# Kernel optimization log

Hardware: AMD Instinct MI355X
Metric: run time of the kernel (lower is better)

The kernel has to match this reference:

```python
import jax, jax.numpy as jnp
import numpy as np

B, H, L, D = 8, 16, 1024, 64


def setup_inputs() -> dict:
    key = jax.random.key(0)
    kq, kk, kv, kb, km = jax.random.split(key, 5)
    q = jax.random.normal(kq, (B, H, L, D), dtype=jnp.float32)
    k = jax.random.normal(kk, (B, H, L, D), dtype=jnp.float32)
    v = jax.random.normal(kv, (B, H, L, D), dtype=jnp.float32)
    # relative-position bias, broadcast over batch
    bias = jax.random.normal(kb, (1, H, L, L), dtype=jnp.float32)
    # variable-length padding mask: each sequence has length in [L//2, L]
    lengths = jax.random.randint(km, (B,), L // 2, L + 1)
    mask = jnp.arange(L)[None, :] < lengths[:, None]  # [B, L] bool
    return {"q": q, "k": k, "v": v, "mask": mask, "bias": bias}


def reference(q, k, v, mask, bias):
    # dots: [b h m n]; NOTE: source computes self.scale but never applies it
    dots = jnp.einsum('bhmd,bhnd->bhmn', q, k) + bias
    # mask[:, None, None, :] & mask[:, None, :, None]
    m2 = mask[:, None, None, :] & mask[:, None, :, None]  # [b 1 m n]
    neg = jnp.finfo(dots.dtype).min
    probs = jax.nn.softmax(jnp.where(m2, dots, neg), axis=-1)
    probs = jnp.where(m2, probs, jnp.zeros((), dtype=probs.dtype))  # XSoftmax zeroing
    # dropout is identity in eval mode
    context = jnp.einsum('bhmn,bhnd->bhmd', probs, v)
    b, h, m, d = context.shape
    return context.transpose(0, 2, 1, 3).reshape(b, m, h * d)  # [b m (h d)]
```

## Files before the change

### kernel.cpp

```cpp
#include <hip/hip_runtime.h>
#include <hip/hip_bf16.h>

#define B_ 8
#define H_ 16
#define L_ 1024
#define D_ 64

typedef __attribute__((ext_vector_type(8))) short short8;
typedef __attribute__((ext_vector_type(4))) short short4v;
typedef __attribute__((ext_vector_type(4))) float floatx4;

__device__ inline short bf16s(float f) {
    union { float f; unsigned u; } un; un.f = f;
    unsigned u = un.u;
    u += 0x7FFFu + ((u >> 16) & 1u);
    return (short)(u >> 16);
}
__device__ inline float bf16f(unsigned short u) {
    union { unsigned u; float f; } un; un.u = ((unsigned)u) << 16;
    return un.f;
}

__device__ inline floatx4 mfma16(short8 a, short8 b, floatx4 c) {
    return __builtin_amdgcn_mfma_f32_16x16x32_bf16(a, b, c, 0, 0, 0);
}

#define KSTR 72
#define VSTR 40
#define PSTR 40
#define KPL (32 * KSTR)
#define VPL (64 * VSTR)
#define PPL (16 * PSTR)

__launch_bounds__(256, 4)
__global__ void prep_kernel(const float* __restrict__ k,
                            const float* __restrict__ v,
                            unsigned short* __restrict__ khi,
                            unsigned short* __restrict__ klo,
                            unsigned short* __restrict__ vth) {
    __shared__ alignas(16) short vt[64 * 72];
    const int bid = blockIdx.x;
    const int kt  = bid & 15;
    const int h   = (bid >> 4) & 15;
    const int b   = bid >> 8;
    const int tid = threadIdx.x;
    const size_t base = ((size_t)(b * H_ + h) * L_ + kt * 64) * D_;

    #pragma unroll
    for (int i = 0; i < 4; i++) {
        const int idx = (i * 256 + tid) * 4;
        const float4 f = *(const float4*)(k + base + idx);
        short4v hi, lo;
        hi[0] = bf16s(f.x); lo[0] = bf16s(f.x - bf16f((unsigned short)hi[0]));
        hi[1] = bf16s(f.y); lo[1] = bf16s(f.y - bf16f((unsigned short)hi[1]));
        hi[2] = bf16s(f.z); lo[2] = bf16s(f.z - bf16f((unsigned short)hi[2]));
        hi[3] = bf16s(f.w); lo[3] = bf16s(f.w - bf16f((unsigned short)hi[3]));
        *(short4v*)(khi + base + idx) = hi;
        *(short4v*)(klo + base + idx) = lo;
    }

    #pragma unroll
    for (int i = 0; i < 4; i++) {
        const int idx = (i * 256 + tid) * 4;
        const int key = idx >> 6;
        const int d0  = idx & 63;
        const float4 f = *(const float4*)(v + base + idx);
        vt[(d0 + 0) * 72 + key] = bf16s(f.x);
        vt[(d0 + 1) * 72 + key] = bf16s(f.y);
        vt[(d0 + 2) * 72 + key] = bf16s(f.z);
        vt[(d0 + 3) * 72 + key] = bf16s(f.w);
    }
    __syncthreads();
    #pragma unroll
    for (int i = 0; i < 2; i++) {
        const int s = i * 2048 + tid * 8;
        const int d = s >> 6;
        const int kk = s & 63;
        short8 r = *(const short8*)&vt[d * 72 + kk];
        *(short8*)(vth + ((size_t)((b * H_ + h) * D_) + d) * L_ + kt * 64 + kk) = r;
    }
}

__launch_bounds__(256, 2)
__global__ void attn_fast(const float* __restrict__ q,
                          const unsigned short* __restrict__ khi,
                          const unsigned short* __restrict__ klo,
                          const unsigned short* __restrict__ vth,
                          const void* __restrict__ mask,
                          const float* __restrict__ bias,
                          float* __restrict__ out) {
    __shared__ alignas(16) short lds_k[2 * 2 * 2 * KPL];
    __shared__ alignas(16) short lds_vt[2 * 2 * VPL];
    __shared__ alignas(16) short lds_p[4 * PPL];
    __shared__ int s_len;

    const int bid  = blockIdx.x;
    const int b    = (bid >> 3) & 7;
    const int p_   = ((bid >> 6) << 3) | (bid & 7);
    const int h    = p_ >> 4;
    const int mt   = p_ & 15;
    const int tid  = threadIdx.x;
    const int wave = tid >> 6;
    const int lane = tid & 63;
    const int l16  = lane & 15;
    const int quad = lane >> 4;
    short* lds_pw = lds_p + wave * PPL;

    if (tid == 0) s_len = 0;
    __syncthreads();
    {
        const unsigned char* mb = (const unsigned char*)mask;
        int fmt;
        if (mb[0] == 1 && mb[1] != 0)      fmt = 0;
        else if (mb[0] == 1)               fmt = 1;
        else if (mb[1] != 0)               fmt = 2;
        else                               fmt = 1;
        int s = 0;
        if (fmt == 0) {
            const unsigned char* r = mb + b * L_;
            #pragma unroll
            for (int i = 0; i < 4; i++) s += (r[tid * 4 + i] != 0);
        } else if (fmt == 1) {
            const unsigned int* r = (const unsigned int*)mask + b * L_;
            #pragma unroll
            for (int i = 0; i < 4; i++) s += (r[tid * 4 + i] != 0u);
        } else {
            const unsigned short* r = (const unsigned short*)mask + b * L_;
            #pragma unroll
            for (int i = 0; i < 4; i++) s += (r[tid * 4 + i] != 0);
        }
        #pragma unroll
        for (int off = 32; off; off >>= 1) s += __shfl_down(s, off);
        if (lane == 0) atomicAdd(&s_len, s);
    }
    __syncthreads();
    const int len = s_len;

    const int m_base = mt * 64 + wave * 16;
    const float* qp = q + ((size_t)((b * H_ + h) * L_) + (m_base + l16)) * D_;
    short8 qh[2], ql[2];
    #pragma unroll
    for (int c = 0; c < 2; c++)
        #pragma unroll
        for (int j = 0; j < 8; j++) {
            float x = qp[c * 32 + quad * 8 + j];
            short hh = bf16s(x);
            qh[c][j] = hh;
            ql[c][j] = bf16s(x - bf16f((unsigned short)hh));
        }

    floatx4 acc[4];
    float l_p[4];
    #pragma unroll
    for (int c = 0; c < 4; c++) { acc[c][0] = acc[c][1] = acc[c][2] = acc[c][3] = 0.f; }
    #pragma unroll
    for (int r = 0; r < 4; r++) l_p[r] = 0.f;

    const size_t kvoff = (size_t)((b * H_ + h) * L_) * D_;
    const size_t vtoff = (size_t)((b * H_ + h) * D_) * L_;
    const float* bias_base = bias + (size_t)h * L_ * L_
                           + (size_t)(m_base + quad * 4) * L_ + l16;

    const int ntiles = (len + 31) >> 5;
    const int npairs = (ntiles + 1) >> 1;

    const int key_s = tid >> 3;
    const int d_s   = (tid & 7) * 8;
    const int dv    = tid >> 2;
    const int k8v   = (tid & 3) * 8;

    short8 khA, klA, vvA, khB, klB, vvB;
    short8 pfA, pfB;
    short8 vfA0, vfA1, vfA2, vfA3, vfB0, vfB1, vfB2, vfB3;

    {
        const size_t ksrc = kvoff + (size_t)tid * 8;
        khA = *(const short8*)(khi + ksrc);
        klA = *(const short8*)(klo + ksrc);
        khB = *(const short8*)(khi + ksrc + 32 * D_);
        klB = *(const short8*)(klo + ksrc + 32 * D_);
        vvA = *(const short8*)(vth + vtoff + (size_t)dv * L_ + k8v);
        vvB = *(const short8*)(vth + vtoff + (size_t)dv * L_ + 32 + k8v);
        short* kA = lds_k;
        short* kB = lds_k + 2 * KPL;
        *(short8*)&kA[key_s * KSTR + d_s] = khA;
        *(short8*)&kA[KPL + key_s * KSTR + d_s] = klA;
        *(short8*)&kB[key_s * KSTR + d_s] = khB;
        *(short8*)&kB[KPL + key_s * KSTR + d_s] = klB;
        *(short8*)&lds_vt[dv * VSTR + k8v] = vvA;
        *(short8*)&lds_vt[VPL + dv * VSTR + k8v] = vvB;
    }
    __syncthreads();

    for (int p = 0; p < npairs; p++) {
        const int n0  = p * 64;
        const int par = p & 1;
        short* kbA = lds_k + (par * 2 + 0) * (2 * KPL);
        short* kbB = lds_k + (par * 2 + 1) * (2 * KPL);
        short* vbA = lds_vt + (par * 2 + 0) * VPL;
        short* vbB = lds_vt + (par * 2 + 1) * VPL;
        const bool pfetch = (p + 1 < npairs);

        if (p > 0) {
            __builtin_amdgcn_s_setprio(1);
            acc[0] = mfma16(pfA, vfA0, acc[0]);
            acc[1] = mfma16(pfA, vfA1, acc[1]);
            acc[2] = mfma16(pfA, vfA2, acc[2]);
            acc[3] = mfma16(pfA, vfA3, acc[3]);
            acc[0] = mfma16(pfB, vfB0, acc[0]);
            acc[1] = mfma16(pfB, vfB1, acc[1]);
            acc[2] = mfma16(pfB, vfB2, acc[2]);
            acc[3] = mfma16(pfB, vfB3, acc[3]);
            __builtin_amdgcn_s_setprio(0);
        }

        if (pfetch) {
            const size_t ksrc = kvoff + (size_t)(n0 + 64) * D_ + (size_t)tid * 8;
            khA = *(const short8*)(khi + ksrc);
            klA = *(const short8*)(klo + ksrc);
            khB = *(const short8*)(khi + ksrc + 32 * D_);
            klB = *(const short8*)(klo + ksrc + 32 * D_);
            vvA = *(const short8*)(vth + vtoff + (size_t)dv * L_ + (n0 + 64) + k8v);
            vvB = *(const short8*)(vth + vtoff + (size_t)dv * L_ + (n0 + 96) + k8v);
        }

        float bc[16];
        #pragma unroll
        for (int r = 0; r < 4; r++) {
            bc[2 * r]         = bias_base[(size_t)r * L_ + n0];
            bc[2 * r + 1]     = bias_base[(size_t)r * L_ + n0 + 16];
            bc[8 + 2 * r]     = bias_base[(size_t)r * L_ + n0 + 32];
            bc[8 + 2 * r + 1] = bias_base[(size_t)r * L_ + n0 + 48];
        }

        vfA0 = *(const short8*)&vbA[(0 * 16 + l16) * VSTR + quad * 8];
        vfA1 = *(const short8*)&vbA[(1 * 16 + l16) * VSTR + quad * 8];
        vfA2 = *(const short8*)&vbA[(2 * 16 + l16) * VSTR + quad * 8];
        vfA3 = *(const short8*)&vbA[(3 * 16 + l16) * VSTR + quad * 8];
        vfB0 = *(const short8*)&vbB[(0 * 16 + l16) * VSTR + quad * 8];
        vfB1 = *(const short8*)&vbB[(1 * 16 + l16) * VSTR + quad * 8];
        vfB2 = *(const short8*)&vbB[(2 * 16 + l16) * VSTR + quad * 8];
        vfB3 = *(const short8*)&vbB[(3 * 16 + l16) * VSTR + quad * 8];

        floatx4 s0a, s1a, s0b, s1b;
        s0a[0]=s0a[1]=s0a[2]=s0a[3]=0.f;
        s1a[0]=s1a[1]=s1a[2]=s1a[3]=0.f;
        s0b[0]=s0b[1]=s0b[2]=s0b[3]=0.f;
        s1b[0]=s1b[1]=s1b[2]=s1b[3]=0.f;
        __builtin_amdgcn_s_setprio(1);
        #pragma unroll
        for (int c = 0; c < 2; c++) {
            const int o0 = l16 * KSTR + c * 32 + quad * 8;
            const int o1 = (16 + l16) * KSTR + c * 32 + quad * 8;
            short8 a0h = *(const short8*)&kbA[o0];
            short8 a1h = *(const short8*)&kbA[o1];
            short8 a0l = *(const short8*)&kbA[KPL + o0];
            short8 a1l = *(const short8*)&kbA[KPL + o1];
            short8 b0h = *(const short8*)&kbB[o0];
            short8 b1h = *(const short8*)&kbB[o1];
            short8 b0l = *(const short8*)&kbB[KPL + o0];
            short8 b1l = *(const short8*)&kbB[KPL + o1];
            s0a = mfma16(qh[c], a0h, s0a);
            s0b = mfma16(qh[c], b0h, s0b);
            s1a = mfma16(qh[c], a1h, s1a);
            s1b = mfma16(qh[c], b1h, s1b);
            s0a = mfma16(ql[c], a0h, s0a);
            s0b = mfma16(ql[c], b0h, s0b);
            s1a = mfma16(ql[c], a1h, s1a);
            s1b = mfma16(ql[c], b1h, s1b);
            s0a = mfma16(qh[c], a0l, s0a);
            s0b = mfma16(qh[c], b0l, s0b);
            s1a = mfma16(qh[c], a1l, s1a);
            s1b = mfma16(qh[c], b1l, s1b);
        }
        __builtin_amdgcn_s_setprio(0);

        #pragma unroll
        for (int r = 0; r < 4; r++) {
            s0a[r] += bc[2 * r];     s1a[r] += bc[2 * r + 1];
            s0b[r] += bc[8 + 2 * r]; s1b[r] += bc[8 + 2 * r + 1];
        }
        if (n0 + l16      >= len) { s0a[0]=s0a[1]=s0a[2]=s0a[3] = -1e30f; }
        if (n0 + 16 + l16 >= len) { s1a[0]=s1a[1]=s1a[2]=s1a[3] = -1e30f; }
        if (n0 + 32 + l16 >= len) { s0b[0]=s0b[1]=s0b[2]=s0b[3] = -1e30f; }
        if (n0 + 48 + l16 >= len) { s1b[0]=s1b[1]=s1b[2]=s1b[3] = -1e30f; }

        #pragma unroll
        for (int r = 0; r < 4; r++) {
            const float p0 = __expf(fminf(s0a[r], 60.f));
            const float p1 = __expf(fminf(s1a[r], 60.f));
            l_p[r] += p0 + p1;
            const int row = quad * 4 + r;
            lds_pw[row * PSTR + l16]      = bf16s(p0);
            lds_pw[row * PSTR + 16 + l16] = bf16s(p1);
        }
        pfA = *(const short8*)&lds_pw[l16 * PSTR + quad * 8];
        #pragma unroll
        for (int r = 0; r < 4; r++) {
            const float p0 = __expf(fminf(s0b[r], 60.f));
            const float p1 = __expf(fminf(s1b[r], 60.f));
            l_p[r] += p0 + p1;
            const int row = quad * 4 + r;
            lds_pw[row * PSTR + l16]      = bf16s(p0);
            lds_pw[row * PSTR + 16 + l16] = bf16s(p1);
        }
        pfB = *(const short8*)&lds_pw[l16 * PSTR + quad * 8];

        if (pfetch) {
            const int par2 = par ^ 1;
            short* kA2 = lds_k + (par2 * 2 + 0) * (2 * KPL);
            short* kB2 = lds_k + (par2 * 2 + 1) * (2 * KPL);
            short* vA2 = lds_vt + (par2 * 2 + 0) * VPL;
            short* vB2 = lds_vt + (par2 * 2 + 1) * VPL;
            *(short8*)&kA2[key_s * KSTR + d_s] = khA;
            *(short8*)&kA2[KPL + key_s * KSTR + d_s] = klA;
            *(short8*)&kB2[key_s * KSTR + d_s] = khB;
            *(short8*)&kB2[KPL + key_s * KSTR + d_s] = klB;
            *(short8*)&vA2[dv * VSTR + k8v] = vvA;
            *(short8*)&vB2[dv * VSTR + k8v] = vvB;
        }
        __syncthreads();
    }

    {
        __builtin_amdgcn_s_setprio(1);
        acc[0] = mfma16(pfA, vfA0, acc[0]);
        acc[1] = mfma16(pfA, vfA1, acc[1]);
        acc[2] = mfma16(pfA, vfA2, acc[2]);
        acc[3] = mfma16(pfA, vfA3, acc[3]);
        acc[0] = mfma16(pfB, vfB0, acc[0]);
        acc[1] = mfma16(pfB, vfB1, acc[1]);
        acc[2] = mfma16(pfB, vfB2, acc[2]);
        acc[3] = mfma16(pfB, vfB3, acc[3]);
        __builtin_amdgcn_s_setprio(0);
    }

    #pragma unroll
    for (int r = 0; r < 4; r++) {
        float ls = l_p[r];
        #pragma unroll
        for (int off = 8; off; off >>= 1) ls += __shfl_xor(ls, off);
        const int mg = m_base + quad * 4 + r;
        const bool valid = (mg < len);
        const float invl = (ls > 0.f) ? (1.0f / ls) : 0.f;
        float* op = out + (size_t)(b * L_ + mg) * (H_ * D_) + h * D_;
        #pragma unroll
        for (int c = 0; c < 4; c++)
            op[c * 16 + l16] = valid ? acc[c][r] * invl : 0.f;
    }
}

__launch_bounds__(256, 4)
__global__ void attn_fallback(const float* __restrict__ q,
                              const float* __restrict__ k,
                              const float* __restrict__ v,
                              const void* __restrict__ mask,
                              const float* __restrict__ bias,
                              float* __restrict__ out) {
    __shared__ alignas(16) short lds_k[2 * KPL];
    __shared__ alignas(16) short lds_vt[2 * VPL];
    __shared__ alignas(16) short lds_p[4 * 2 * PPL];
    __shared__ int s_len;

    const int bid  = blockIdx.x;
    const int mt   = bid & 15;
    const int h    = (bid >> 4) & 15;
    const int b    = bid >> 8;
    const int tid  = threadIdx.x;
    const int wave = tid >> 6;
    const int lane = tid & 63;
    const int l16  = lane & 15;
    const int quad = lane >> 4;
    short* lds_pw = lds_p + wave * (2 * PPL);

    if (tid == 0) s_len = 0;
    __syncthreads();
    {
        const unsigned char* mb = (const unsigned char*)mask;
        int fmt;
        if (mb[0] == 1 && mb[1] != 0)      fmt = 0;
        else if (mb[0] == 1)               fmt = 1;
        else if (mb[1] != 0)               fmt = 2;
        else                               fmt = 1;
        int s = 0;
        if (fmt == 0) {
            const unsigned char* r = mb + b * L_;
            for (int i = 0; i < 4; i++) s += (r[tid * 4 + i] != 0);
        } else if (fmt == 1) {
            const unsigned int* r = (const unsigned int*)mask + b * L_;
            for (int i = 0; i < 4; i++) s += (r[tid * 4 + i] != 0u);
        } else {
            const unsigned short* r = (const unsigned short*)mask + b * L_;
            for (int i = 0; i < 4; i++) s += (r[tid * 4 + i] != 0);
        }
        for (int off = 32; off; off >>= 1) s += __shfl_down(s, off);
        if (lane == 0) atomicAdd(&s_len, s);
    }
    __syncthreads();
    const int len = s_len;

    const int m_base = mt * 64 + wave * 16;
    const float* qp = q + ((size_t)((b * H_ + h) * L_) + (m_base + l16)) * D_;
    short8 qh[2], ql[2];
    for (int c = 0; c < 2; c++)
        for (int j = 0; j < 8; j++) {
            float x = qp[c * 32 + quad * 8 + j];
            short hh = bf16s(x);
            qh[c][j] = hh;
            ql[c][j] = bf16s(x - bf16f((unsigned short)hh));
        }

    floatx4 acc[4];
    float m_i[4], l_i[4];
    for (int c = 0; c < 4; c++) { acc[c][0]=acc[c][1]=acc[c][2]=acc[c][3]=0.f; }
    for (int r = 0; r < 4; r++) { m_i[r] = -1e30f; l_i[r] = 0.f; }

    const size_t kvoff = (size_t)((b * H_ + h) * L_) * D_;
    const size_t boff0 = (size_t)h * L_ * L_;
    const int ntiles = (len + 31) >> 5;

    for (int kt = 0; kt < ntiles; kt++) {
        const int n0 = kt * 32;
        __syncthreads();
        {
            const int e0  = tid * 8;
            const int key = e0 >> 6;
            const int d0  = e0 & 63;
            const float* ksrc = k + kvoff + (size_t)(n0 + key) * D_ + d0;
            const float* vsrc = v + kvoff + (size_t)(n0 + key) * D_ + d0;
            short* kdh = &lds_k[key * KSTR + d0];
            for (int i = 0; i < 8; i++) {
                float x = ksrc[i];
                short hh = bf16s(x);
                kdh[i]       = hh;
                kdh[KPL + i] = bf16s(x - bf16f((unsigned short)hh));
            }
            for (int i = 0; i < 8; i++) {
                float x = vsrc[i];
                short hh = bf16s(x);
                lds_vt[(d0 + i) * VSTR + key]       = hh;
                lds_vt[VPL + (d0 + i) * VSTR + key] = bf16s(x - bf16f((unsigned short)hh));
            }
        }
        __syncthreads();

        floatx4 s0, s1;
        s0[0]=s0[1]=s0[2]=s0[3]=0.f;
        s1[0]=s1[1]=s1[2]=s1[3]=0.f;
        for (int c = 0; c < 2; c++) {
            const int o0 = l16 * KSTR + c * 32 + quad * 8;
            const int o1 = (16 + l16) * KSTR + c * 32 + quad * 8;
            short8 k0h = *(const short8*)&lds_k[o0];
            short8 k1h = *(const short8*)&lds_k[o1];
            short8 k0l = *(const short8*)&lds_k[KPL + o0];
            short8 k1l = *(const short8*)&lds_k[KPL + o1];
            s0 = mfma16(qh[c], k0h, s0);
            s0 = mfma16(ql[c], k0h, s0);
            s0 = mfma16(qh[c], k0l, s0);
            s1 = mfma16(qh[c], k1h, s1);
            s1 = mfma16(ql[c], k1h, s1);
            s1 = mfma16(qh[c], k1l, s1);
        }

        for (int r = 0; r < 4; r++) {
            const float* bp = bias + boff0 + (size_t)(m_base + quad * 4 + r) * L_ + n0;
            s0[r] += bp[l16];
            s1[r] += bp[16 + l16];
        }
        if (n0 + l16      >= len) { s0[0]=s0[1]=s0[2]=s0[3] = -1e30f; }
        if (n0 + 16 + l16 >= len) { s1[0]=s1[1]=s1[2]=s1[3] = -1e30f; }

        for (int r = 0; r < 4; r++) {
            float mx = fmaxf(s0[r], s1[r]);
            for (int off = 8; off; off >>= 1) mx = fmaxf(mx, __shfl_xor(mx, off));
            const float mnew  = fmaxf(m_i[r], mx);
            const float alpha = __expf(m_i[r] - mnew);
            const float p0 = __expf(s0[r] - mnew);
            const float p1 = __expf(s1[r] - mnew);
            float ps = p0 + p1;
            for (int off = 8; off; off >>= 1) ps += __shfl_xor(ps, off);
            l_i[r] = l_i[r] * alpha + ps;
            m_i[r] = mnew;
            for (int c = 0; c < 4; c++) acc[c][r] *= alpha;
            const int row = quad * 4 + r;
            short h0 = bf16s(p0), h1 = bf16s(p1);
            lds_pw[row * PSTR + l16]      = h0;
            lds_pw[row * PSTR + 16 + l16] = h1;
            lds_pw[PPL + row * PSTR + l16]      = bf16s(p0 - bf16f((unsigned short)h0));
            lds_pw[PPL + row * PSTR + 16 + l16] = bf16s(p1 - bf16f((unsigned short)h1));
        }

        short8 pfh = *(const short8*)&lds_pw[l16 * PSTR + quad * 8];
        short8 pfl = *(const short8*)&lds_pw[PPL + l16 * PSTR + quad * 8];
        for (int c = 0; c < 4; c++) {
            const int vo = (c * 16 + l16) * VSTR + quad * 8;
            short8 vfh = *(const short8*)&lds_vt[vo];
            short8 vfl = *(const short8*)&lds_vt[VPL + vo];
            acc[c] = mfma16(pfh, vfh, acc[c]);
            acc[c] = mfma16(pfl, vfh, acc[c]);
            acc[c] = mfma16(pfh, vfl, acc[c]);
        }
    }

    for (int r = 0; r < 4; r++) {
        const int mg = m_base + quad * 4 + r;
        const bool valid = (mg < len);
        const float invl = (l_i[r] > 0.f) ? (1.0f / l_i[r]) : 0.f;
        float* op = out + (size_t)(b * L_ + mg) * (H_ * D_) + h * D_;
        for (int c = 0; c < 4; c++)
            op[c * 16 + l16] = valid ? acc[c][r] * invl : 0.f;
    }
}

extern "C" void kernel_launch(void* const* d_in, const int* in_sizes, int n_in,
                              void* d_out, int out_size, void* d_ws, size_t ws_size,
                              hipStream_t stream) {
    const float* q    = (const float*)d_in[0];
    const float* k    = (const float*)d_in[1];
    const float* v    = (const float*)d_in[2];
    const void*  mask = d_in[3];
    const float* bias = (const float*)d_in[4];
    float* out = (float*)d_out;

    const size_t PLANE = (size_t)B_ * H_ * L_ * D_;
    const size_t need  = 3 * PLANE * sizeof(unsigned short);

    dim3 grid(B_ * H_ * (L_ / 64));
    if (ws_size >= need) {
        unsigned short* khi = (unsigned short*)d_ws;
        unsigned short* klo = khi + PLANE;
        unsigned short* vth = klo + PLANE;
        prep_kernel<<<grid, 256, 0, stream>>>(k, v, khi, klo, vth);
        attn_fast<<<grid, 256, 0, stream>>>(q, khi, klo, vth, mask, bias, out);
    } else {
        attn_fallback<<<grid, 256, 0, stream>>>(q, k, v, mask, bias, out);
    }
}
```

Baseline: 290.4 us.

## Use 512-thread blocks covering 128 query rows to share K/V tiles

The attention kernel now runs 8 waves per block, so each block covers 128 query rows and the grid is halved. Each staged 64-key K (hi/lo) and V tile is loaded once per block by all 512 threads and shared by twice as many waves, which halves global-to-LDS traffic per query row. The LDS layout changes to single 64-key buffers with a new V stride. The costs are larger block-wide barriers, fewer blocks in flight, and more LDS per block. Register pressure from the new launch bounds may also become a problem.

```diff
diff --git a/kernel.cpp b/kernel.cpp
--- a/kernel.cpp
+++ b/kernel.cpp
@@ -31,6 +31,9 @@
 #define KPL (32 * KSTR)
 #define VPL (64 * VSTR)
 #define PPL (16 * PSTR)
+#define KPL64 (64 * KSTR)
+#define VSTR2 68
+#define VPL64 (64 * VSTR2)
 
 __launch_bounds__(256, 4)
 __global__ void prep_kernel(const float* __restrict__ k,
@@ -81,7 +84,7 @@
     }
 }
 
-__launch_bounds__(256, 2)
+__launch_bounds__(512, 4)
 __global__ void attn_fast(const float* __restrict__ q,
                           const unsigned short* __restrict__ khi,
                           const unsigned short* __restrict__ klo,
@@ -89,16 +92,16 @@
                           const void* __restrict__ mask,
                           const float* __restrict__ bias,
                           float* __restrict__ out) {
-    __shared__ alignas(16) short lds_k[2 * 2 * 2 * KPL];
-    __shared__ alignas(16) short lds_vt[2 * 2 * VPL];
-    __shared__ alignas(16) short lds_p[4 * PPL];
+    __shared__ alignas(16) short lds_k[2 * 2 * KPL64];
+    __shared__ alignas(16) short lds_vt[2 * VPL64];
+    __shared__ alignas(16) short lds_p[8 * PPL];
     __shared__ int s_len;
 
     const int bid  = blockIdx.x;
     const int b    = (bid >> 3) & 7;
     const int p_   = ((bid >> 6) << 3) | (bid & 7);
-    const int h    = p_ >> 4;
-    const int mt   = p_ & 15;
+    const int h    = p_ >> 3;
+    const int mt2  = p_ & 7;
     const int tid  = threadIdx.x;
     const int wave = tid >> 6;
     const int lane = tid & 63;
@@ -108,7 +111,7 @@
 
     if (tid == 0) s_len = 0;
     __syncthreads();
-    {
+    if (tid < 256) {
         const unsigned char* mb = (const unsigned char*)mask;
         int fmt;
         if (mb[0] == 1 && mb[1] != 0)      fmt = 0;
@@ -136,7 +139,7 @@
     __syncthreads();
     const int len = s_len;
 
-    const int m_base = mt * 64 + wave * 16;
+    const int m_base = mt2 * 128 + wave * 16;
     const float* qp = q + ((size_t)((b * H_ + h) * L_) + (m_base + l16)) * D_;
     short8 qh[2], ql[2];
     #pragma unroll
@@ -166,39 +169,29 @@
 
     const int key_s = tid >> 3;
     const int d_s   = (tid & 7) * 8;
-    const int dv    = tid >> 2;
-    const int k8v   = (tid & 3) * 8;
-
-    short8 khA, klA, vvA, khB, klB, vvB;
+    const int dv    = tid >> 3;
+    const int k8v   = (tid & 7) * 8;
+
+    short8 kh_r, kl_r, vv_r;
     short8 pfA, pfB;
     short8 vfA0, vfA1, vfA2, vfA3, vfB0, vfB1, vfB2, vfB3;
 
     {
         const size_t ksrc = kvoff + (size_t)tid * 8;
-        khA = *(const short8*)(khi + ksrc);
-        klA = *(const short8*)(klo + ksrc);
-        khB = *(const short8*)(khi + ksrc + 32 * D_);
-        klB = *(const short8*)(klo + ksrc + 32 * D_);
-        vvA = *(const short8*)(vth + vtoff + (size_t)dv * L_ + k8v);
-        vvB = *(const short8*)(vth + vtoff + (size_t)dv * L_ + 32 + k8v);
-        short* kA = lds_k;
-        short* kB = lds_k + 2 * KPL;
-        *(short8*)&kA[key_s * KSTR + d_s] = khA;
-        *(short8*)&kA[KPL + key_s * KSTR + d_s] = klA;
-        *(short8*)&kB[key_s * KSTR + d_s] = khB;
-        *(short8*)&kB[KPL + key_s * KSTR + d_s] = klB;
-        *(short8*)&lds_vt[dv * VSTR + k8v] = vvA;
-        *(short8*)&lds_vt[VPL + dv * VSTR + k8v] = vvB;
+        kh_r = *(const short8*)(khi + ksrc);
+        kl_r = *(const short8*)(klo + ksrc);
+        vv_r = *(const short8*)(vth + vtoff + (size_t)dv * L_ + k8v);
+        *(short8*)&lds_k[key_s * KSTR + d_s] = kh_r;
+        *(short8*)&lds_k[KPL64 + key_s * KSTR + d_s] = kl_r;
+        *(short8*)&lds_vt[dv * VSTR2 + k8v] = vv_r;
     }
     __syncthreads();
 
     for (int p = 0; p < npairs; p++) {
         const int n0  = p * 64;
         const int par = p & 1;
-        short* kbA = lds_k + (par * 2 + 0) * (2 * KPL);
-        short* kbB = lds_k + (par * 2 + 1) * (2 * KPL);
-        short* vbA = lds_vt + (par * 2 + 0) * VPL;
-        short* vbB = lds_vt + (par * 2 + 1) * VPL;
+        short* kb = lds_k + par * (2 * KPL64);
+        short* vb = lds_vt + par * VPL64;
         const bool pfetch = (p + 1 < npairs);
 
         if (p > 0) {
@@ -216,12 +209,9 @@
 
         if (pfetch) {
             const size_t ksrc = kvoff + (size_t)(n0 + 64) * D_ + (size_t)tid * 8;
-            khA = *(const short8*)(khi + ksrc);
-            klA = *(const short8*)(klo + ksrc);
-            khB = *(const short8*)(khi + ksrc + 32 * D_);
-            klB = *(const short8*)(klo + ksrc + 32 * D_);
-            vvA = *(const short8*)(vth + vtoff + (size_t)dv * L_ + (n0 + 64) + k8v);
-            vvB = *(const short8*)(vth + vtoff + (size_t)dv * L_ + (n0 + 96) + k8v);
+            kh_r = *(const short8*)(khi + ksrc);
+            kl_r = *(const short8*)(klo + ksrc);
+            vv_r = *(const short8*)(vth + vtoff + (size_t)dv * L_ + (n0 + 64) + k8v);
         }
 
         float bc[16];
@@ -233,14 +223,14 @@
             bc[8 + 2 * r + 1] = bias_base[(size_t)r * L_ + n0 + 48];
         }
 
-        vfA0 = *(const short8*)&vbA[(0 * 16 + l16) * VSTR + quad * 8];
-        vfA1 = *(const short8*)&vbA[(1 * 16 + l16) * VSTR + quad * 8];
-        vfA2 = *(const short8*)&vbA[(2 * 16 + l16) * VSTR + quad * 8];
-        vfA3 = *(const short8*)&vbA[(3 * 16 + l16) * VSTR + quad * 8];
-        vfB0 = *(const short8*)&vbB[(0 * 16 + l16) * VSTR + quad * 8];
-        vfB1 = *(const short8*)&vbB[(1 * 16 + l16) * VSTR + quad * 8];
-        vfB2 = *(const short8*)&vbB[(2 * 16 + l16) * VSTR + quad * 8];
-        vfB3 = *(const short8*)&vbB[(3 * 16 + l16) * VSTR + quad * 8];
+        vfA0 = *(const short8*)&vb[(0 * 16 + l16) * VSTR2 + quad * 8];
+        vfA1 = *(const short8*)&vb[(1 * 16 + l16) * VSTR2 + quad * 8];
+        vfA2 = *(const short8*)&vb[(2 * 16 + l16) * VSTR2 + quad * 8];
+        vfA3 = *(const short8*)&vb[(3 * 16 + l16) * VSTR2 + quad * 8];
+        vfB0 = *(const short8*)&vb[(0 * 16 + l16) * VSTR2 + 32 + quad * 8];
+        vfB1 = *(const short8*)&vb[(1 * 16 + l16) * VSTR2 + 32 + quad * 8];
+        vfB2 = *(const short8*)&vb[(2 * 16 + l16) * VSTR2 + 32 + quad * 8];
+        vfB3 = *(const short8*)&vb[(3 * 16 + l16) * VSTR2 + 32 + quad * 8];
 
         floatx4 s0a, s1a, s0b, s1b;
         s0a[0]=s0a[1]=s0a[2]=s0a[3]=0.f;
@@ -250,16 +240,18 @@
         __builtin_amdgcn_s_setprio(1);
         #pragma unroll
         for (int c = 0; c < 2; c++) {
-            const int o0 = l16 * KSTR + c * 32 + quad * 8;
-            const int o1 = (16 + l16) * KSTR + c * 32 + quad * 8;
-            short8 a0h = *(const short8*)&kbA[o0];
-            short8 a1h = *(const short8*)&kbA[o1];
-            short8 a0l = *(const short8*)&kbA[KPL + o0];
-            short8 a1l = *(const short8*)&kbA[KPL + o1];
-            short8 b0h = *(const short8*)&kbB[o0];
-            short8 b1h = *(const short8*)&kbB[o1];
-            short8 b0l = *(const short8*)&kbB[KPL + o0];
-            short8 b1l = *(const short8*)&kbB[KPL + o1];
+            const int o0  = l16 * KSTR + c * 32 + quad * 8;
+            const int o1  = (16 + l16) * KSTR + c * 32 + quad * 8;
+            const int o0b = (32 + l16) * KSTR + c * 32 + quad * 8;
+            const int o1b = (48 + l16) * KSTR + c * 32 + quad * 8;
+            short8 a0h = *(const short8*)&kb[o0];
+            short8 a1h = *(const short8*)&kb[o1];
+            short8 a0l = *(const short8*)&kb[KPL64 + o0];
+            short8 a1l = *(const short8*)&kb[KPL64 + o1];
+            short8 b0h = *(const short8*)&kb[o0b];
+            short8 b1h = *(const short8*)&kb[o1b];
+            short8 b0l = *(const short8*)&kb[KPL64 + o0b];
+            short8 b1l = *(const short8*)&kb[KPL64 + o1b];
             s0a = mfma16(qh[c], a0h, s0a);
             s0b = mfma16(qh[c], b0h, s0b);
             s1a = mfma16(qh[c], a1h, s1a);
@@ -308,16 +300,11 @@
 
         if (pfetch) {
             const int par2 = par ^ 1;
-            short* kA2 = lds_k + (par2 * 2 + 0) * (2 * KPL);
-            short* kB2 = lds_k + (par2 * 2 + 1) * (2 * KPL);
-            short* vA2 = lds_vt + (par2 * 2 + 0) * VPL;
-            short* vB2 = lds_vt + (par2 * 2 + 1) * VPL;
-            *(short8*)&kA2[key_s * KSTR + d_s] = khA;
-            *(short8*)&kA2[KPL + key_s * KSTR + d_s] = klA;
-            *(short8*)&kB2[key_s * KSTR + d_s] = khB;
-            *(short8*)&kB2[KPL + key_s * KSTR + d_s] = klB;
-            *(short8*)&vA2[dv * VSTR + k8v] = vvA;
-            *(short8*)&vB2[dv * VSTR + k8v] = vvB;
+            short* kb2 = lds_k + par2 * (2 * KPL64);
+            short* vb2 = lds_vt + par2 * VPL64;
+            *(short8*)&kb2[key_s * KSTR + d_s] = kh_r;
+            *(short8*)&kb2[KPL64 + key_s * KSTR + d_s] = kl_r;
+            *(short8*)&vb2[dv * VSTR2 + k8v] = vv_r;
         }
         __syncthreads();
     }
@@ -525,14 +512,13 @@
     const size_t PLANE = (size_t)B_ * H_ * L_ * D_;
     const size_t need  = 3 * PLANE * sizeof(unsigned short);
 
-    dim3 grid(B_ * H_ * (L_ / 64));
     if (ws_size >= need) {
         unsigned short* khi = (unsigned short*)d_ws;
         unsigned short* klo = khi + PLANE;
         unsigned short* vth = klo + PLANE;
-        prep_kernel<<<grid, 256, 0, stream>>>(k, v, khi, klo, vth);
-        attn_fast<<<grid, 256, 0, stream>>>(q, khi, klo, vth, mask, bias, out);
+        prep_kernel<<<dim3(B_ * H_ * (L_ / 64)), 256, 0, stream>>>(k, v, khi, klo, vth);
+        attn_fast<<<dim3(B_ * H_ * (L_ / 128)), 512, 0, stream>>>(q, khi, klo, vth, mask, bias, out);
     } else {
-        attn_fallback<<<grid, 256, 0, stream>>>(q, k, v, mask, bias, out);
-    }
-}
+        attn_fallback<<<dim3(B_ * H_ * (L_ / 64)), 256, 0, stream>>>(q, k, v, mask, bias, out);
+    }
+}
```

Result: slower. 479.4 us (+65.1%).
